# Optimization experiments

Measured on AMD Instinct MI355X. Metric: run time of the kernel, lower is better.

The kernel has to match this reference:

```python
import jax, jax.numpy as jnp
import numpy as np

BS, NF, MAXC, NLOC = 8, 32, 4, 65536
DELTA_VAR, DELTA_DIST = 0.5, 1.5
ALPHA, BETA, GAMMA = 1.0, 1.0, 1e-4
K_ACTIVE = 2  # every sample has exactly 2 active clusters (indices 0,1), matching the
              # original code's len(class_index)==2 filter in _cluster_means


def _safe_norm(sq):
    # sqrt of sum-of-squares with a zero-safe gradient (torch.norm subgradient at 0 is 0)
    s = jnp.where(sq > 0, sq, 1.0)
    return jnp.where(sq > 0, jnp.sqrt(s), 0.0)


def setup_inputs() -> dict:
    key = jax.random.key(0)
    k1, k2 = jax.random.split(key)
    inp = jax.random.normal(k1, (BS, NF, NLOC), dtype=jnp.float32)
    labels = jax.random.randint(k2, (BS, NLOC), 0, K_ACTIVE)  # only clusters 0,1 populated
    target = jnp.transpose(jax.nn.one_hot(labels, MAXC, dtype=jnp.float32), (0, 2, 1))  # (BS, MAXC, NLOC)
    n_clusters = jnp.full((BS,), K_ACTIVE, dtype=jnp.int32)
    return {"input": inp, "target": target, "n_clusters": n_clusters}


def reference(input, target, n_clusters):
    nc = n_clusters.astype(jnp.float32)                      # (bs,)
    counts = target.sum(-1)                                  # (bs, maxc) pixels per cluster
    active = counts > 0
    safe_counts = jnp.where(active, counts, 1.0)

    # cluster means: masked segment-mean, zeros for padded/inactive clusters
    sums = jnp.einsum('bfn,bcn->bfc', input, target)          # (bs, nf, maxc)
    means = jnp.where(active[:, None, :], sums / safe_counts[:, None, :], 0.0)

    # variance term: pull embeddings within delta_var of their cluster mean
    diff = input[:, :, None, :] - means[:, :, :, None]        # (bs, nf, maxc, nloc)
    dist = _safe_norm(jnp.sum(diff * diff, axis=1))           # (bs, maxc, nloc) L2 over features
    var = jnp.maximum(dist - DELTA_VAR, 0.0) ** 2 * target
    c_var = jnp.where(active, var.sum(-1) / safe_counts, 0.0)  # per-cluster mean
    l_var = jnp.mean(c_var.sum(-1) / nc)

    # distance term: push cluster means at least 2*delta_dist apart (K_ACTIVE clusters)
    m = means[:, :, :K_ACTIVE]                                # (bs, nf, K)
    d = m[:, :, :, None] - m[:, :, None, :]                   # (bs, nf, K, K)
    dn = _safe_norm(jnp.sum(d * d, axis=1))                   # (bs, K, K)
    margin = 2.0 * DELTA_DIST * (1.0 - jnp.eye(K_ACTIVE, dtype=jnp.float32))
    c_dist = jnp.sum(jnp.maximum(margin - dn, 0.0) ** 2, axis=(1, 2))
    l_dist = jnp.mean(c_dist / (2.0 * nc * (nc - 1.0)))

    # regularization: mean L2 norm of the active cluster means
    l_reg = jnp.mean(jnp.mean(_safe_norm(jnp.sum(m * m, axis=1)), axis=-1))

    return ALPHA * l_var + BETA * l_dist + GAMMA * l_reg
```

## Files before the change

kernel.cpp:

```cpp
#include <hip/hip_runtime.h>
#include <math.h>

#define BS 8
#define NF 32
#define MAXC 4
#define NLOC 65536
#define DELTA_VAR 0.5f
#define DELTA_DIST 1.5f
#define GAMMA 1e-4f

#define WS_COUNTS 0
#define WS_MEANS  32
#define WS_M2     1056
#define WS_VARSUM 1088
#define WS_PART   2112
#define GG 128
#define PART_SZ (BS * GG * 68)

__global__ __launch_bounds__(256, 4) void k_sums(const float* __restrict__ inp,
                                                 const float* __restrict__ tgt,
                                                 float* __restrict__ ws,
                                                 unsigned char* __restrict__ labels) {
  constexpr int CHUNK = NLOC / GG;
  float* part = ws + WS_PART;
  const int b = blockIdx.y;
  const int gx = blockIdx.x;
  const int lane = threadIdx.x & 63;
  const int fg = threadIdx.x >> 6;
  const int n0 = gx * CHUNK;
  const float* inp_b = inp + (size_t)b * NF * NLOC + (size_t)fg * 8 * NLOC;
  const float* tgt_b = tgt + (size_t)b * MAXC * NLOC;

  float r[16];
#pragma unroll
  for (int k = 0; k < 16; ++k) r[k] = 0.f;
  float cnt0 = 0.f;

#pragma unroll
  for (int it = 0; it < CHUNK / 256; ++it) {
    const int n = n0 + it * 256 + lane * 4;
    float4 t0 = *reinterpret_cast<const float4*>(tgt_b + n);
    float4 x[8];
#pragma unroll
    for (int i = 0; i < 8; ++i)
      x[i] = *reinterpret_cast<const float4*>(inp_b + i * NLOC + n);
    if (fg == 0) {
      cnt0 += t0.x + t0.y + t0.z + t0.w;
      uchar4 l4;
      l4.x = t0.x > 0.5f ? 0 : 1;
      l4.y = t0.y > 0.5f ? 0 : 1;
      l4.z = t0.z > 0.5f ? 0 : 1;
      l4.w = t0.w > 0.5f ? 0 : 1;
      *reinterpret_cast<uchar4*>(labels + (size_t)b * NLOC + n) = l4;
    }
#pragma unroll
    for (int i = 0; i < 8; ++i) {
      r[i * 2 + 0] += x[i].x + x[i].y + x[i].z + x[i].w;
      r[i * 2 + 1] += x[i].x * t0.x + x[i].y * t0.y + x[i].z * t0.z + x[i].w * t0.w;
    }
  }

#define BSTEP(m, half)                                      \
  {                                                         \
    _Pragma("unroll") for (int j = 0; j < half; ++j) {      \
      float aa = __shfl_xor(r[j], m, 64);                   \
      float bb = __shfl_xor(r[j + half], m, 64);            \
      r[j] = (lane & m) ? (r[j + half] + bb) : (r[j] + aa); \
    }                                                       \
  }
  BSTEP(32, 8)
  BSTEP(16, 4)
  BSTEP(8, 2)
  BSTEP(4, 1)
#undef BSTEP
  r[0] += __shfl_xor(r[0], 2, 64);
  r[0] += __shfl_xor(r[0], 1, 64);

  __shared__ float pp[68];
  if ((lane & 3) == 0) pp[fg * 16 + (lane >> 2)] = r[0];

  if (fg == 0) {
    cnt0 += __shfl_xor(cnt0, 32, 64);
    cnt0 += __shfl_xor(cnt0, 16, 64);
    cnt0 += __shfl_xor(cnt0, 8, 64);
    cnt0 += __shfl_xor(cnt0, 4, 64);
    cnt0 += __shfl_xor(cnt0, 2, 64);
    cnt0 += __shfl_xor(cnt0, 1, 64);
    if (lane == 0) pp[64] = cnt0;
  }
  __syncthreads();
  if (threadIdx.x < 65)
    part[((size_t)(b * GG + gx)) * 68 + threadIdx.x] = pp[threadIdx.x];
}

__global__ __launch_bounds__(512) void k_reduce(float* __restrict__ ws) {
  const float* part = ws + WS_PART;
  const int b = blockIdx.x;
  const int t = threadIdx.x;
  __shared__ float sbuf[8][64];
  __shared__ float cbuf[GG];
  __shared__ float tbuf[64];
  __shared__ float cnt_s[2];
  __shared__ float m2buf[2][32];
  const float* pb = part + (size_t)b * GG * 68;

  {
    const int rem = t & 63, q = t >> 6;
    float s = 0.f;
    for (int g = q * (GG / 8); g < (q + 1) * (GG / 8); ++g)
      s += pb[(size_t)g * 68 + rem];
    sbuf[q][rem] = s;
  }
  if (t < GG) cbuf[t] = pb[(size_t)t * 68 + 64];
  __syncthreads();
  if (t < 64) {
    float s = 0.f;
#pragma unroll
    for (int q = 0; q < 8; ++q) s += sbuf[q][t];
    tbuf[t] = s;
  }
  if (t == 64) {
    float c = 0.f;
    for (int g = 0; g < GG; ++g) c += cbuf[g];
    cnt_s[0] = c;
    cnt_s[1] = (float)NLOC - c;
  }
  __syncthreads();
  if (t < 32) {
    float sx = tbuf[t * 2], s0 = tbuf[t * 2 + 1];
    float c0 = cnt_s[0], c1 = cnt_s[1];
    float mean0 = c0 > 0.f ? s0 / c0 : 0.f;
    float mean1 = c1 > 0.f ? (sx - s0) / c1 : 0.f;
    ws[WS_MEANS + b * 128 + t * 4 + 0] = mean0;
    ws[WS_MEANS + b * 128 + t * 4 + 1] = mean1;
    ws[WS_MEANS + b * 128 + t * 4 + 2] = 0.f;
    ws[WS_MEANS + b * 128 + t * 4 + 3] = 0.f;
    m2buf[0][t] = mean0 * mean0;
    m2buf[1][t] = mean1 * mean1;
  }
  __syncthreads();
  if (t < 2) {
    float m2 = 0.f;
#pragma unroll
    for (int f = 0; f < 32; ++f) m2 += m2buf[t][f];
    ws[WS_M2 + b * 4 + t] = m2;
  } else if (t < 4) {
    ws[WS_M2 + b * 4 + t] = 0.f;
  } else if (t < 8) {
    const int c = t - 4;
    ws[WS_COUNTS + b * 4 + c] = c < 2 ? cnt_s[c] : 0.f;
  } else if (t < 12) {
    ws[WS_VARSUM + (b * 4 + (t - 8)) * 32] = 0.f;
  }
}

__global__ __launch_bounds__(256, 4) void k_var(const float* __restrict__ inp,
                                                const unsigned char* __restrict__ labels,
                                                float* __restrict__ ws) {
  const int b = blockIdx.y;
  __shared__ float2 m_lds[NF];
  __shared__ float m2_s[2];
  __shared__ float vred[4][2];
  if (threadIdx.x < NF) {
    const float* mb = ws + WS_MEANS + b * 128 + threadIdx.x * 4;
    m_lds[threadIdx.x] = make_float2(mb[0], mb[1]);
  }
  if (threadIdx.x < 2) m2_s[threadIdx.x] = ws[WS_M2 + b * 4 + threadIdx.x];
  __syncthreads();

  const int n = blockIdx.x * 512 + threadIdx.x * 2;
  const float* inp_b = inp + (size_t)b * NF * NLOC;
  const uchar2 lab = *reinterpret_cast<const uchar2*>(labels + (size_t)b * NLOC + n);

  float s2x = 0.f, s2y = 0.f;
  float d0x = 0.f, d0y = 0.f, d1x = 0.f, d1y = 0.f;
#pragma unroll
  for (int f = 0; f < NF; ++f) {
    float2 x = *reinterpret_cast<const float2*>(inp_b + f * NLOC + n);
    float2 m = m_lds[f];
    s2x += x.x * x.x; s2y += x.y * x.y;
    d0x += x.x * m.x; d0y += x.y * m.x;
    d1x += x.x * m.y; d1y += x.y * m.y;
  }

  float vacc0 = 0.f, vacc1 = 0.f;
  {
    const float d = lab.x ? d1x : d0x;
    const float m2 = lab.x ? m2_s[1] : m2_s[0];
    float sq = s2x - 2.f * d + m2;
    float dist = sq > 0.f ? sqrtf(sq) : 0.f;
    float v = fmaxf(dist - DELTA_VAR, 0.f);
    float vv = v * v;
    vacc0 += lab.x ? 0.f : vv;
    vacc1 += lab.x ? vv : 0.f;
  }
  {
    const float d = lab.y ? d1y : d0y;
    const float m2 = lab.y ? m2_s[1] : m2_s[0];
    float sq = s2y - 2.f * d + m2;
    float dist = sq > 0.f ? sqrtf(sq) : 0.f;
    float v = fmaxf(dist - DELTA_VAR, 0.f);
    float vv = v * v;
    vacc0 += lab.y ? 0.f : vv;
    vacc1 += lab.y ? vv : 0.f;
  }

  const int lane = threadIdx.x & 63;
  const int wave = threadIdx.x >> 6;
  float aa = __shfl_xor(vacc0, 32, 64);
  float bb = __shfl_xor(vacc1, 32, 64);
  float u = (lane & 32) ? (vacc1 + bb) : (vacc0 + aa);
  u += __shfl_xor(u, 16, 64);
  u += __shfl_xor(u, 8, 64);
  u += __shfl_xor(u, 4, 64);
  u += __shfl_xor(u, 2, 64);
  u += __shfl_xor(u, 1, 64);
  if ((lane & 31) == 0) vred[wave][lane >> 5] = u;
  __syncthreads();
  if (threadIdx.x < 2) {
    const int c = threadIdx.x;
    float s = vred[0][c] + vred[1][c] + vred[2][c] + vred[3][c];
    atomicAdd(&ws[WS_VARSUM + (b * 4 + c) * 32], s);
  }
}

__global__ void k_final(const float* __restrict__ ws,
                        const int* __restrict__ n_clusters,
                        float* __restrict__ out) {
  const int lane = threadIdx.x;
  float total = 0.f;
  if (lane < BS) {
    const int b = lane;
    const float nc = (float)n_clusters[b];
    float sv = 0.f;
    for (int c = 0; c < MAXC; ++c) {
      float cntc = ws[WS_COUNTS + b * 4 + c];
      if (cntc > 0.f) sv += ws[WS_VARSUM + (b * 4 + c) * 32] / cntc;
    }
    float l_var = sv / nc;
    float d2 = 0.f, n0s = 0.f, n1s = 0.f;
    for (int f = 0; f < NF; ++f) {
      float m0 = ws[WS_MEANS + (b * NF + f) * 4 + 0];
      float m1 = ws[WS_MEANS + (b * NF + f) * 4 + 1];
      float df = m0 - m1;
      d2 += df * df;
      n0s += m0 * m0;
      n1s += m1 * m1;
    }
    float dn = d2 > 0.f ? sqrtf(d2) : 0.f;
    float h = fmaxf(2.f * DELTA_DIST - dn, 0.f);
    float c_dist = 2.f * h * h;
    float l_dist = c_dist / (2.f * nc * (nc - 1.f));
    float r0 = n0s > 0.f ? sqrtf(n0s) : 0.f;
    float r1 = n1s > 0.f ? sqrtf(n1s) : 0.f;
    float l_reg = 0.5f * (r0 + r1);
    total = l_var + l_dist + GAMMA * l_reg;
  }
#pragma unroll
  for (int m = 1; m < 8; m <<= 1) total += __shfl_xor(total, m, 64);
  if (lane == 0) out[0] = total / (float)BS;
}

extern "C" void kernel_launch(void* const* d_in, const int* in_sizes, int n_in,
                              void* d_out, int out_size, void* d_ws, size_t ws_size,
                              hipStream_t stream) {
  const float* inp = (const float*)d_in[0];
  const float* tgt = (const float*)d_in[1];
  const int* ncl = (const int*)d_in[2];
  float* out = (float*)d_out;
  float* ws = (float*)d_ws;
  unsigned char* labels = (unsigned char*)(ws + WS_PART + PART_SZ);

  k_sums<<<dim3(GG, BS), 256, 0, stream>>>(inp, tgt, ws, labels);
  k_reduce<<<BS, 512, 0, stream>>>(ws);
  k_var<<<dim3(128, BS), 256, 0, stream>>>(inp, labels, ws);
  k_final<<<1, 64, 0, stream>>>(ws, ncl, out);
}
```

Baseline: 35.87 us.

## Fuse reduce and final kernels into var kernel with last-block finalization

```diff
diff --git a/kernel.cpp b/kernel.cpp
--- a/kernel.cpp
+++ b/kernel.cpp
@@ -3,33 +3,33 @@
 
 #define BS 8
 #define NF 32
-#define MAXC 4
 #define NLOC 65536
 #define DELTA_VAR 0.5f
 #define DELTA_DIST 1.5f
 #define GAMMA 1e-4f
+#define G 128
+#define CHUNK 512
 
 #define WS_COUNTS 0
-#define WS_MEANS  32
-#define WS_M2     1056
-#define WS_VARSUM 1088
-#define WS_PART   2112
-#define GG 128
-#define PART_SZ (BS * GG * 68)
+#define WS_MEANS  16
+#define WS_VARSUM 528
+#define WS_CTR    1040
+#define WS_PART   1072
+#define WS_LABELS (1072 + BS * G * 68)
 
 __global__ __launch_bounds__(256, 4) void k_sums(const float* __restrict__ inp,
                                                  const float* __restrict__ tgt,
                                                  float* __restrict__ ws,
                                                  unsigned char* __restrict__ labels) {
-  constexpr int CHUNK = NLOC / GG;
   float* part = ws + WS_PART;
   const int b = blockIdx.y;
   const int gx = blockIdx.x;
-  const int lane = threadIdx.x & 63;
-  const int fg = threadIdx.x >> 6;
+  const int tid = threadIdx.x;
+  const int lane = tid & 63;
+  const int fg = tid >> 6;
   const int n0 = gx * CHUNK;
   const float* inp_b = inp + (size_t)b * NF * NLOC + (size_t)fg * 8 * NLOC;
-  const float* tgt_b = tgt + (size_t)b * MAXC * NLOC;
+  const float* t0_b = tgt + (size_t)b * 4 * NLOC;
 
   float r[16];
 #pragma unroll
@@ -39,7 +39,7 @@
 #pragma unroll
   for (int it = 0; it < CHUNK / 256; ++it) {
     const int n = n0 + it * 256 + lane * 4;
-    float4 t0 = *reinterpret_cast<const float4*>(tgt_b + n);
+    float4 t0 = *reinterpret_cast<const float4*>(t0_b + n);
     float4 x[8];
 #pragma unroll
     for (int i = 0; i < 8; ++i)
@@ -89,176 +89,162 @@
     if (lane == 0) pp[64] = cnt0;
   }
   __syncthreads();
-  if (threadIdx.x < 65)
-    part[((size_t)(b * GG + gx)) * 68 + threadIdx.x] = pp[threadIdx.x];
-}
-
-__global__ __launch_bounds__(512) void k_reduce(float* __restrict__ ws) {
-  const float* part = ws + WS_PART;
-  const int b = blockIdx.x;
-  const int t = threadIdx.x;
-  __shared__ float sbuf[8][64];
-  __shared__ float cbuf[GG];
-  __shared__ float tbuf[64];
-  __shared__ float cnt_s[2];
-  __shared__ float m2buf[2][32];
-  const float* pb = part + (size_t)b * GG * 68;
-
-  {
-    const int rem = t & 63, q = t >> 6;
-    float s = 0.f;
-    for (int g = q * (GG / 8); g < (q + 1) * (GG / 8); ++g)
-      s += pb[(size_t)g * 68 + rem];
-    sbuf[q][rem] = s;
-  }
-  if (t < GG) cbuf[t] = pb[(size_t)t * 68 + 64];
-  __syncthreads();
-  if (t < 64) {
-    float s = 0.f;
-#pragma unroll
-    for (int q = 0; q < 8; ++q) s += sbuf[q][t];
-    tbuf[t] = s;
-  }
-  if (t == 64) {
-    float c = 0.f;
-    for (int g = 0; g < GG; ++g) c += cbuf[g];
-    cnt_s[0] = c;
-    cnt_s[1] = (float)NLOC - c;
-  }
-  __syncthreads();
-  if (t < 32) {
-    float sx = tbuf[t * 2], s0 = tbuf[t * 2 + 1];
-    float c0 = cnt_s[0], c1 = cnt_s[1];
-    float mean0 = c0 > 0.f ? s0 / c0 : 0.f;
-    float mean1 = c1 > 0.f ? (sx - s0) / c1 : 0.f;
-    ws[WS_MEANS + b * 128 + t * 4 + 0] = mean0;
-    ws[WS_MEANS + b * 128 + t * 4 + 1] = mean1;
-    ws[WS_MEANS + b * 128 + t * 4 + 2] = 0.f;
-    ws[WS_MEANS + b * 128 + t * 4 + 3] = 0.f;
-    m2buf[0][t] = mean0 * mean0;
-    m2buf[1][t] = mean1 * mean1;
-  }
-  __syncthreads();
-  if (t < 2) {
-    float m2 = 0.f;
-#pragma unroll
-    for (int f = 0; f < 32; ++f) m2 += m2buf[t][f];
-    ws[WS_M2 + b * 4 + t] = m2;
-  } else if (t < 4) {
-    ws[WS_M2 + b * 4 + t] = 0.f;
-  } else if (t < 8) {
-    const int c = t - 4;
-    ws[WS_COUNTS + b * 4 + c] = c < 2 ? cnt_s[c] : 0.f;
-  } else if (t < 12) {
-    ws[WS_VARSUM + (b * 4 + (t - 8)) * 32] = 0.f;
-  }
+  if (tid < 65) part[((size_t)(b * G + gx)) * 68 + tid] = pp[tid];
+  if (gx == 0 && tid < 2) ws[WS_VARSUM + (b * 2 + tid) * 32] = 0.f;
+  if (gx == 0 && b == 0 && tid == 0)
+    *reinterpret_cast<unsigned int*>(ws + WS_CTR) = 0u;
 }
 
 __global__ __launch_bounds__(256, 4) void k_var(const float* __restrict__ inp,
                                                 const unsigned char* __restrict__ labels,
-                                                float* __restrict__ ws) {
+                                                const int* __restrict__ ncl,
+                                                float* __restrict__ ws,
+                                                float* __restrict__ out) {
   const int b = blockIdx.y;
+  const int gx = blockIdx.x;
+  const int tid = threadIdx.x;
+  const int lane = tid & 63;
+  const int fg = tid >> 6;
+
+  __shared__ float sbuf[4][64];
+  __shared__ float tbuf[64];
+  __shared__ float cbuf[G];
+  __shared__ float cnt_s[2];
   __shared__ float2 m_lds[NF];
-  __shared__ float m2_s[2];
   __shared__ float vred[4][2];
-  if (threadIdx.x < NF) {
-    const float* mb = ws + WS_MEANS + b * 128 + threadIdx.x * 4;
-    m_lds[threadIdx.x] = make_float2(mb[0], mb[1]);
-  }
-  if (threadIdx.x < 2) m2_s[threadIdx.x] = ws[WS_M2 + b * 4 + threadIdx.x];
-  __syncthreads();
-
-  const int n = blockIdx.x * 512 + threadIdx.x * 2;
-  const float* inp_b = inp + (size_t)b * NF * NLOC;
-  const uchar2 lab = *reinterpret_cast<const uchar2*>(labels + (size_t)b * NLOC + n);
-
-  float s2x = 0.f, s2y = 0.f;
-  float d0x = 0.f, d0y = 0.f, d1x = 0.f, d1y = 0.f;
-#pragma unroll
-  for (int f = 0; f < NF; ++f) {
-    float2 x = *reinterpret_cast<const float2*>(inp_b + f * NLOC + n);
-    float2 m = m_lds[f];
-    s2x += x.x * x.x; s2y += x.y * x.y;
-    d0x += x.x * m.x; d0y += x.y * m.x;
-    d1x += x.x * m.y; d1y += x.y * m.y;
-  }
-
-  float vacc0 = 0.f, vacc1 = 0.f;
+  __shared__ int last_flag;
+
   {
-    const float d = lab.x ? d1x : d0x;
-    const float m2 = lab.x ? m2_s[1] : m2_s[0];
-    float sq = s2x - 2.f * d + m2;
-    float dist = sq > 0.f ? sqrtf(sq) : 0.f;
-    float v = fmaxf(dist - DELTA_VAR, 0.f);
-    float vv = v * v;
-    vacc0 += lab.x ? 0.f : vv;
-    vacc1 += lab.x ? vv : 0.f;
-  }
+    const float* pb = ws + WS_PART + (size_t)b * G * 68;
+    const int q = tid >> 6, rem = tid & 63;
+    float s = 0.f;
+    for (int g2 = q * 32; g2 < q * 32 + 32; ++g2) s += pb[(size_t)g2 * 68 + rem];
+    sbuf[q][rem] = s;
+    if (tid < G) cbuf[tid] = pb[(size_t)tid * 68 + 64];
+    __syncthreads();
+    if (tid < 64) {
+      tbuf[tid] = sbuf[0][tid] + sbuf[1][tid] + sbuf[2][tid] + sbuf[3][tid];
+      float c = cbuf[tid] + cbuf[tid + 64];
+      c += __shfl_xor(c, 32, 64);
+      c += __shfl_xor(c, 16, 64);
+      c += __shfl_xor(c, 8, 64);
+      c += __shfl_xor(c, 4, 64);
+      c += __shfl_xor(c, 2, 64);
+      c += __shfl_xor(c, 1, 64);
+      if (tid == 0) {
+        cnt_s[0] = c;
+        cnt_s[1] = (float)NLOC - c;
+      }
+    }
+    __syncthreads();
+    if (tid < 32) {
+      const int f = tid;
+      float sx = tbuf[f * 2], s0 = tbuf[f * 2 + 1];
+      float c0 = cnt_s[0], c1 = cnt_s[1];
+      float m0 = c0 > 0.f ? s0 / c0 : 0.f;
+      float m1 = c1 > 0.f ? (sx - s0) / c1 : 0.f;
+      m_lds[f] = make_float2(m0, m1);
+      if (gx == 0) {
+        ws[WS_MEANS + (b * NF + f) * 2 + 0] = m0;
+        ws[WS_MEANS + (b * NF + f) * 2 + 1] = m1;
+        if (f < 2) ws[WS_COUNTS + b * 2 + f] = cnt_s[f];
+      }
+    }
+    __syncthreads();
+  }
+
   {
-    const float d = lab.y ? d1y : d0y;
-    const float m2 = lab.y ? m2_s[1] : m2_s[0];
-    float sq = s2y - 2.f * d + m2;
-    float dist = sq > 0.f ? sqrtf(sq) : 0.f;
-    float v = fmaxf(dist - DELTA_VAR, 0.f);
-    float vv = v * v;
-    vacc0 += lab.y ? 0.f : vv;
-    vacc1 += lab.y ? vv : 0.f;
-  }
-
-  const int lane = threadIdx.x & 63;
-  const int wave = threadIdx.x >> 6;
-  float aa = __shfl_xor(vacc0, 32, 64);
-  float bb = __shfl_xor(vacc1, 32, 64);
-  float u = (lane & 32) ? (vacc1 + bb) : (vacc0 + aa);
-  u += __shfl_xor(u, 16, 64);
-  u += __shfl_xor(u, 8, 64);
-  u += __shfl_xor(u, 4, 64);
-  u += __shfl_xor(u, 2, 64);
-  u += __shfl_xor(u, 1, 64);
-  if ((lane & 31) == 0) vred[wave][lane >> 5] = u;
-  __syncthreads();
-  if (threadIdx.x < 2) {
-    const int c = threadIdx.x;
-    float s = vred[0][c] + vred[1][c] + vred[2][c] + vred[3][c];
-    atomicAdd(&ws[WS_VARSUM + (b * 4 + c) * 32], s);
-  }
-}
-
-__global__ void k_final(const float* __restrict__ ws,
-                        const int* __restrict__ n_clusters,
-                        float* __restrict__ out) {
-  const int lane = threadIdx.x;
-  float total = 0.f;
-  if (lane < BS) {
-    const int b = lane;
-    const float nc = (float)n_clusters[b];
-    float sv = 0.f;
-    for (int c = 0; c < MAXC; ++c) {
-      float cntc = ws[WS_COUNTS + b * 4 + c];
-      if (cntc > 0.f) sv += ws[WS_VARSUM + (b * 4 + c) * 32] / cntc;
-    }
-    float l_var = sv / nc;
-    float d2 = 0.f, n0s = 0.f, n1s = 0.f;
+    const float* inp_b = inp + (size_t)b * NF * NLOC;
+    const int n = gx * CHUNK + tid * 2;
+    const uchar2 lab = *reinterpret_cast<const uchar2*>(labels + (size_t)b * NLOC + n);
+    float ax = 0.f, ay = 0.f;
+#pragma unroll
     for (int f = 0; f < NF; ++f) {
-      float m0 = ws[WS_MEANS + (b * NF + f) * 4 + 0];
-      float m1 = ws[WS_MEANS + (b * NF + f) * 4 + 1];
-      float df = m0 - m1;
-      d2 += df * df;
-      n0s += m0 * m0;
-      n1s += m1 * m1;
-    }
-    float dn = d2 > 0.f ? sqrtf(d2) : 0.f;
-    float h = fmaxf(2.f * DELTA_DIST - dn, 0.f);
-    float c_dist = 2.f * h * h;
-    float l_dist = c_dist / (2.f * nc * (nc - 1.f));
-    float r0 = n0s > 0.f ? sqrtf(n0s) : 0.f;
-    float r1 = n1s > 0.f ? sqrtf(n1s) : 0.f;
-    float l_reg = 0.5f * (r0 + r1);
-    total = l_var + l_dist + GAMMA * l_reg;
-  }
-#pragma unroll
-  for (int m = 1; m < 8; m <<= 1) total += __shfl_xor(total, m, 64);
-  if (lane == 0) out[0] = total / (float)BS;
+      float2 x = *reinterpret_cast<const float2*>(inp_b + f * NLOC + n);
+      float2 m = m_lds[f];
+      float mx = lab.x ? m.y : m.x;
+      float my = lab.y ? m.y : m.x;
+      float dx = x.x - mx, dy = x.y - my;
+      ax += dx * dx;
+      ay += dy * dy;
+    }
+    float vx = fmaxf(sqrtf(ax) - DELTA_VAR, 0.f);
+    float vy = fmaxf(sqrtf(ay) - DELTA_VAR, 0.f);
+    vx *= vx;
+    vy *= vy;
+    float vacc0 = (lab.x ? 0.f : vx) + (lab.y ? 0.f : vy);
+    float vacc1 = (lab.x ? vx : 0.f) + (lab.y ? vy : 0.f);
+
+    float aa = __shfl_xor(vacc0, 32, 64);
+    float bb = __shfl_xor(vacc1, 32, 64);
+    float u = (lane & 32) ? (vacc1 + bb) : (vacc0 + aa);
+    u += __shfl_xor(u, 16, 64);
+    u += __shfl_xor(u, 8, 64);
+    u += __shfl_xor(u, 4, 64);
+    u += __shfl_xor(u, 2, 64);
+    u += __shfl_xor(u, 1, 64);
+    if ((lane & 31) == 0) vred[fg][lane >> 5] = u;
+    __syncthreads();
+    if (tid < 2) {
+      float s = vred[0][tid] + vred[1][tid] + vred[2][tid] + vred[3][tid];
+      atomicAdd(&ws[WS_VARSUM + (b * 2 + tid) * 32], s);
+    }
+  }
+
+  __threadfence();
+  __syncthreads();
+  if (tid == 0) {
+    unsigned int* ctr = reinterpret_cast<unsigned int*>(ws + WS_CTR);
+    unsigned int old =
+        __hip_atomic_fetch_add(ctr, 1u, __ATOMIC_ACQ_REL, __HIP_MEMORY_SCOPE_AGENT);
+    last_flag = (old == (unsigned int)(G * BS - 1)) ? 1 : 0;
+  }
+  __syncthreads();
+  if (!last_flag) return;
+
+  __shared__ float eme[BS * NF * 2];
+  __shared__ float ecnt[BS * 2];
+  __shared__ float evs[BS * 2];
+  for (int k = tid; k < BS * NF * 2; k += 256)
+    eme[k] = __hip_atomic_load(ws + WS_MEANS + k, __ATOMIC_RELAXED,
+                               __HIP_MEMORY_SCOPE_AGENT);
+  if (tid < BS * 2) {
+    ecnt[tid] = __hip_atomic_load(ws + WS_COUNTS + tid, __ATOMIC_RELAXED,
+                                  __HIP_MEMORY_SCOPE_AGENT);
+    evs[tid] = __hip_atomic_load(ws + WS_VARSUM + tid * 32, __ATOMIC_RELAXED,
+                                 __HIP_MEMORY_SCOPE_AGENT);
+  }
+  __syncthreads();
+  if (tid < 64) {
+    float total = 0.f;
+    if (tid < BS) {
+      const int bb2 = tid;
+      const float nc = (float)ncl[bb2];
+      float c0 = ecnt[bb2 * 2 + 0], c1 = ecnt[bb2 * 2 + 1];
+      float v0 = evs[bb2 * 2 + 0], v1 = evs[bb2 * 2 + 1];
+      float sv = (c0 > 0.f ? v0 / c0 : 0.f) + (c1 > 0.f ? v1 / c1 : 0.f);
+      float l_var = sv / nc;
+      float d2 = 0.f, n0s = 0.f, n1s = 0.f;
+      for (int f = 0; f < NF; ++f) {
+        float m0 = eme[(bb2 * NF + f) * 2 + 0];
+        float m1 = eme[(bb2 * NF + f) * 2 + 1];
+        float df = m0 - m1;
+        d2 += df * df;
+        n0s += m0 * m0;
+        n1s += m1 * m1;
+      }
+      float dn = d2 > 0.f ? sqrtf(d2) : 0.f;
+      float h = fmaxf(2.f * DELTA_DIST - dn, 0.f);
+      float l_dist = 2.f * h * h / (2.f * nc * (nc - 1.f));
+      float r0 = n0s > 0.f ? sqrtf(n0s) : 0.f;
+      float r1 = n1s > 0.f ? sqrtf(n1s) : 0.f;
+      float l_reg = 0.5f * (r0 + r1);
+      total = l_var + l_dist + GAMMA * l_reg;
+    }
+#pragma unroll
+    for (int m = 1; m < 8; m <<= 1) total += __shfl_xor(total, m, 64);
+    if (tid == 0) out[0] = total / (float)BS;
+  }
 }
 
 extern "C" void kernel_launch(void* const* d_in, const int* in_sizes, int n_in,
@@ -269,10 +255,8 @@
   const int* ncl = (const int*)d_in[2];
   float* out = (float*)d_out;
   float* ws = (float*)d_ws;
-  unsigned char* labels = (unsigned char*)(ws + WS_PART + PART_SZ);
-
-  k_sums<<<dim3(GG, BS), 256, 0, stream>>>(inp, tgt, ws, labels);
-  k_reduce<<<BS, 512, 0, stream>>>(ws);
-  k_var<<<dim3(128, BS), 256, 0, stream>>>(inp, labels, ws);
-  k_final<<<1, 64, 0, stream>>>(ws, ncl, out);
+  unsigned char* labels = (unsigned char*)(ws + WS_LABELS);
+
+  k_sums<<<dim3(G, BS), 256, 0, stream>>>(inp, tgt, ws, labels);
+  k_var<<<dim3(G, BS), 256, 0, stream>>>(inp, labels, ncl, ws, out);
 }
```

Result: slower. 138.4 us (+285.7%).
